# Performance work log

Hardware: AMD Instinct MI355X
Metric: run time of the kernel (lower is better)

Reference implementation:

```python
import jax, jax.numpy as jnp
import numpy as np

N = 50000      # nodes
E = 800000     # edges
IN = 128       # in_channels
HID = 64       # hidden_channels (out per head)
H = 4          # heads
ED = 64        # edge_dim
HC = H * HID   # concat output width


def segment_softmax(logits, seg, num_segments):
    # logits: [E, H], softmax over edges sharing the same destination node
    m = jax.ops.segment_max(logits, seg, num_segments=num_segments)
    m = jnp.where(jnp.isfinite(m), m, 0.0)
    e = jnp.exp(logits - m[seg])
    s = jax.ops.segment_sum(e, seg, num_segments=num_segments)
    return e / (s[seg] + 1e-16)


def gatv2_layer(x, src, dst, edge_attr, Wl, bl, Wr, br, We, att, bias):
    # GATv2Conv (PyG, concat=True, negative_slope=0.2), dropout off (eval)
    Hh, C = att.shape
    xl = (x @ Wl + bl).reshape(-1, Hh, C)   # [N,H,C] source transform
    xr = (x @ Wr + br).reshape(-1, Hh, C)   # [N,H,C] target transform
    ee = (edge_attr @ We).reshape(-1, Hh, C)  # [E,H,C]
    m = jax.nn.leaky_relu(xl[src] + xr[dst] + ee, 0.2)  # [E,H,C]
    logits = jnp.einsum('ehc,hc->eh', m, att)           # [E,H]
    alpha = segment_softmax(logits, dst, x.shape[0])    # [E,H]
    out = jax.ops.segment_sum(alpha[:, :, None] * xl[src], dst,
                              num_segments=x.shape[0])  # [N,H,C]
    return out.reshape(x.shape[0], Hh * C) + bias


def setup_inputs() -> dict:
    key = jax.random.key(0)
    ks = jax.random.split(key, 20)
    g = lambda k, shape, s=0.05: (jax.random.normal(k, shape, jnp.float32) * s)
    inp = {
        'x': jax.random.normal(ks[0], (N, IN), jnp.float32),
        'edge_index': jax.random.randint(ks[1], (2, E), 0, N, dtype=jnp.int32),
        'edge_attr': jax.random.normal(ks[2], (E, ED), jnp.float32),
        # layer 1: in_channels -> heads*hidden
        'Wl1': g(ks[3], (IN, HC)), 'bl1': jnp.zeros((HC,), jnp.float32),
        'Wr1': g(ks[4], (IN, HC)), 'br1': jnp.zeros((HC,), jnp.float32),
        'We1': g(ks[5], (ED, HC)),
        'att1': g(ks[6], (H, HID)), 'bias1': jnp.zeros((HC,), jnp.float32),
        # layer 2: heads*hidden -> heads*hidden
        'Wl2': g(ks[7], (HC, HC)), 'bl2': jnp.zeros((HC,), jnp.float32),
        'Wr2': g(ks[8], (HC, HC)), 'br2': jnp.zeros((HC,), jnp.float32),
        'We2': g(ks[9], (ED, HC)),
        'att2': g(ks[10], (H, HID)), 'bias2': jnp.zeros((HC,), jnp.float32),
    }
    return inp


def reference(x, edge_index, edge_attr,
              Wl1, bl1, Wr1, br1, We1, att1, bias1,
              Wl2, bl2, Wr2, br2, We2, att2, bias2):
    src, dst = edge_index[0], edge_index[1]
    h1 = gatv2_layer(x, src, dst, edge_attr, Wl1, bl1, Wr1, br1, We1, att1, bias1)
    h2 = gatv2_layer(h1, src, dst, edge_attr, Wl2, bl2, Wr2, br2, We2, att2, bias2)
    return h2
```

## Files before the change

kernel.cpp:

```cpp
#include <hip/hip_runtime.h>
#include <math.h>

#define NN 50000
#define NE 800000

#define LRELU(v) fmaxf((v), 0.2f * (v))

typedef __attribute__((ext_vector_type(4))) float f32x4;
typedef __attribute__((ext_vector_type(8))) short bf16x8;

static __device__ __forceinline__ unsigned short f2bf(float f) {
  union { float f; unsigned int i; } c; c.f = f;
  unsigned int r = c.i + 0x7fff + ((c.i >> 16) & 1);
  return (unsigned short)(r >> 16);
}
static __device__ __forceinline__ float bflo(unsigned int u) {
  union { unsigned int i; float f; } c; c.i = u << 16; return c.f;
}
static __device__ __forceinline__ float bfhi(unsigned int u) {
  union { unsigned int i; float f; } c; c.i = u & 0xffff0000u; return c.f;
}

__global__ __launch_bounds__(256)
void conv_all(const float* __restrict__ We1, unsigned short* __restrict__ wef1,
              const float* __restrict__ We2, unsigned short* __restrict__ wef2,
              const float* __restrict__ Wl1, unsigned short* __restrict__ wlf1,
              const float* __restrict__ Wr1, unsigned short* __restrict__ wrf1,
              const float* __restrict__ Wl2, unsigned short* __restrict__ wlf2,
              const float* __restrict__ Wr2, unsigned short* __restrict__ wrf2) {
  const int y = blockIdx.y;
  const int g = blockIdx.x * 256 + threadIdx.x;
  if (y < 2) {
    if (g >= 16384) return;
    const float* We = y ? We2 : We1;
    unsigned short* wef = y ? wef2 : wef1;
    const int j = g & 7;
    const int l = (g >> 3) & 63;
    const int t = g >> 9;
    const int n = t & 15, half = t >> 4;
    const int k = half * 32 + (l >> 4) * 8 + j;
    const int c = ((l & 15) >> 2) * 64 + n * 4 + (l & 3);
    wef[g] = f2bf(We[(size_t)k * 256 + c]);
  } else {
    const int K = (y < 4) ? 128 : 256;
    if (g >= K * 256) return;
    const float* W = (y == 2) ? Wl1 : (y == 3) ? Wr1 : (y == 4) ? Wl2 : Wr2;
    unsigned short* wf = (y == 2) ? wlf1 : (y == 3) ? wrf1
                       : (y == 4) ? wlf2 : wrf2;
    const int j = g & 7;
    const int l = (g >> 3) & 63;
    const int fn = g >> 9;
    const int n = fn & 15, ks = fn >> 4;
    const int k = ks * 32 + (l >> 4) * 8 + j;
    const int c = n * 16 + (l & 15);
    wf[g] = f2bf(W[(size_t)k * 256 + c]);
  }
}

template <int KS, int BF>
__global__ __launch_bounds__(256)
void gemm_mfma4(const void* __restrict__ Av,
                const unsigned short* __restrict__ wf0,
                const float* __restrict__ b0, unsigned short* __restrict__ out0,
                const unsigned short* __restrict__ wf1,
                const float* __restrict__ b1, unsigned short* __restrict__ out1) {
  const int mat = blockIdx.y & 1;
  const int nh  = blockIdx.y >> 1;
  const unsigned short* wf = mat ? wf1 : wf0;
  const float* bias        = mat ? b1 : b0;
  unsigned short* outb     = mat ? out1 : out0;

  const int tid = threadIdx.x;
  const int w = tid >> 6, l = tid & 63;
  const int lid = l & 15, lg = l >> 4;
  const int row  = blockIdx.x * 64 + w * 16 + lid;
  const bool rowok = row < NN;
  const int rowv = rowok ? row : NN - 1;
  const int K = KS * 32;

  bf16x8 bfr[KS];
  if (BF) {
    const unsigned short* A = (const unsigned short*)Av;
    const unsigned short* ap = A + (size_t)rowv * K + lg * 8;
#pragma unroll
    for (int ks = 0; ks < KS; ++ks)
      bfr[ks] = *(const bf16x8*)(ap + ks * 32);
  } else {
    const float* A = (const float*)Av;
    const float* ap = A + (size_t)rowv * K + lg * 8;
#pragma unroll
    for (int ks = 0; ks < KS; ++ks) {
      const float4 v0 = *(const float4*)(ap + ks * 32);
      const float4 v1 = *(const float4*)(ap + ks * 32 + 4);
      bf16x8 b;
      b[0]=f2bf(v0.x); b[1]=f2bf(v0.y); b[2]=f2bf(v0.z); b[3]=f2bf(v0.w);
      b[4]=f2bf(v1.x); b[5]=f2bf(v1.y); b[6]=f2bf(v1.z); b[7]=f2bf(v1.w);
      bfr[ks] = b;
    }
  }

  f32x4 acc[8];
#pragma unroll
  for (int n8 = 0; n8 < 8; ++n8) acc[n8] = (f32x4){0.f, 0.f, 0.f, 0.f};

#pragma unroll
  for (int ks = 0; ks < KS; ++ks)
#pragma unroll
    for (int n8 = 0; n8 < 8; ++n8) {
      const int n = nh * 8 + n8;
      const bf16x8 a = *(const bf16x8*)(wf + ((size_t)(ks * 16 + n) * 64 + l) * 8);
      acc[n8] = __builtin_amdgcn_mfma_f32_16x16x32_bf16(a, bfr[ks], acc[n8], 0, 0, 0);
    }

  if (rowok) {
#pragma unroll
    for (int n8 = 0; n8 < 8; ++n8) {
      const int c0 = (nh * 8 + n8) * 16 + lg * 4;
      const float4 bv = *(const float4*)(bias + c0);
      ushort4 o;
      o.x = f2bf(acc[n8][0] + bv.x); o.y = f2bf(acc[n8][1] + bv.y);
      o.z = f2bf(acc[n8][2] + bv.z); o.w = f2bf(acc[n8][3] + bv.w);
      *(ushort4*)(outb + (size_t)row * 256 + c0) = o;
    }
  }
}

__global__ __launch_bounds__(256)
void dst_hist(const int* __restrict__ dst, int* __restrict__ cnt) {
  const int e = blockIdx.x * 256 + threadIdx.x;
  if (e < NE) atomicAdd(&cnt[dst[e]], 1);
}

__global__ __launch_bounds__(1024)
void scan_bsum(const int* __restrict__ cnt, int* __restrict__ bsum, int n) {
  __shared__ int wsum[16];
  const int tid = threadIdx.x;
  const int lane = tid & 63, wid = tid >> 6;
  const int i = blockIdx.x * 1024 + tid;
  int v = (i < n) ? cnt[i] : 0;
#pragma unroll
  for (int off = 32; off >= 1; off >>= 1) v += __shfl_xor(v, off);
  if (lane == 0) wsum[wid] = v;
  __syncthreads();
  if (tid == 0) {
    int s = 0;
#pragma unroll
    for (int k = 0; k < 16; ++k) s += wsum[k];
    bsum[blockIdx.x] = s;
  }
}

__global__ __launch_bounds__(64)
void scan_bsum_scan(int* __restrict__ bsum, int* __restrict__ row_start,
                    int nb, int n) {
  const int lane = threadIdx.x;
  const int v = (lane < nb) ? bsum[lane] : 0;
  int incl = v;
#pragma unroll
  for (int off = 1; off < 64; off <<= 1) {
    const int t = __shfl_up(incl, off);
    if (lane >= off) incl += t;
  }
  if (lane < nb) bsum[lane] = incl - v;
  if (lane == 63) row_start[n] = incl;
}

__global__ __launch_bounds__(1024)
void scan_apply(int* __restrict__ cnt, const int* __restrict__ bsum,
                int* __restrict__ row_start, int n) {
  __shared__ int wsum[16];
  __shared__ int woff[16];
  const int tid = threadIdx.x;
  const int lane = tid & 63, wid = tid >> 6;
  const int i = blockIdx.x * 1024 + tid;
  const int v = (i < n) ? cnt[i] : 0;
  int incl = v;
#pragma unroll
  for (int off = 1; off < 64; off <<= 1) {
    const int t = __shfl_up(incl, off);
    if (lane >= off) incl += t;
  }
  if (lane == 63) wsum[wid] = incl;
  __syncthreads();
  if (wid == 0) {
    const int s = (lane < 16) ? wsum[lane] : 0;
    int si = s;
#pragma unroll
    for (int off = 1; off < 16; off <<= 1) {
      const int t = __shfl_up(si, off);
      if (lane >= off) si += t;
    }
    if (lane < 16) woff[lane] = si - s;
  }
  __syncthreads();
  if (i < n) {
    const int excl = bsum[blockIdx.x] + woff[wid] + incl - v;
    row_start[i] = excl;
    cnt[i] = excl;
  }
}

__global__ __launch_bounds__(256)
void bucket_fill(const int* __restrict__ src, const int* __restrict__ dst,
                 int* __restrict__ cur, int* __restrict__ eid,
                 int* __restrict__ ssrc, int* __restrict__ sdst) {
  const int e = blockIdx.x * 256 + threadIdx.x;
  if (e < NE) {
    const int d = dst[e];
    const int p = atomicAdd(&cur[d], 1);
    eid[p] = e;
    ssrc[p] = src[e];
    sdst[p] = d;
  }
}

__global__ __launch_bounds__(256)
void conv_eab(const float* __restrict__ ea, const int* __restrict__ eid,
              unsigned short* __restrict__ eab) {
  const int g = blockIdx.x * 256 + threadIdx.x;
  const int p = g >> 4, c4 = (g & 15) * 4;
  const int e = eid[p];
  const float4 v = *(const float4*)(ea + (size_t)e * 64 + c4);
  ushort4 o;
  o.x = f2bf(v.x); o.y = f2bf(v.y); o.z = f2bf(v.z); o.w = f2bf(v.w);
  *(ushort4*)(eab + (size_t)p * 64 + c4) = o;
}

template <int EAB>
__global__ __launch_bounds__(128)
void edge_logits_glds(const float* __restrict__ ea,
                      const unsigned short* __restrict__ eab,
                      const unsigned short* __restrict__ wef,
                      const unsigned short* __restrict__ xlb,
                      const unsigned short* __restrict__ xrb,
                      const float* __restrict__ att,
                      const int* __restrict__ eid,
                      const int* __restrict__ ssrc, const int* __restrict__ sdst,
                      float* __restrict__ elog) {
  __shared__ unsigned short sxl[2][16 * 256];

  const int tid = threadIdx.x;
  const int w = tid >> 6, l = tid & 63;
  const int lid = l & 15, lg = l >> 4;
  const int base = (blockIdx.x * 2 + w) * 16;
  const int p = base + lid;

  const int my_s = ssrc[p];

  const int rr = l >> 5;
  const int u_phys = l & 31;
#pragma unroll
  for (int i = 0; i < 8; ++i) {
    const int r = 2 * i + rr;
    const int srow = __shfl(my_s, r);
    const int u = u_phys ^ (r & 7);
    const unsigned short* gsrc = xlb + (size_t)srow * 256 + u * 8;
    __builtin_amdgcn_global_load_lds(
        (const __attribute__((address_space(1))) unsigned int*)gsrc,
        (__attribute__((address_space(3))) unsigned int*)&sxl[w][i * 512],
        16, 0, 0);
  }

  bf16x8 f0, f1;
  if (EAB) {
    f0 = *(const bf16x8*)(eab + (size_t)p * 64 + lg * 8);
    f1 = *(const bf16x8*)(eab + (size_t)p * 64 + 32 + lg * 8);
  } else {
    const int e = eid[p];
    const float* ap = ea + (size_t)e * 64 + lg * 8;
    const float4 v00 = *(const float4*)(ap);
    const float4 v01 = *(const float4*)(ap + 4);
    const float4 v10 = *(const float4*)(ap + 32);
    const float4 v11 = *(const float4*)(ap + 36);
    f0[0]=f2bf(v00.x); f0[1]=f2bf(v00.y); f0[2]=f2bf(v00.z); f0[3]=f2bf(v00.w);
    f0[4]=f2bf(v01.x); f0[5]=f2bf(v01.y); f0[6]=f2bf(v01.z); f0[7]=f2bf(v01.w);
    f1[0]=f2bf(v10.x); f1[1]=f2bf(v10.y); f1[2]=f2bf(v10.z); f1[3]=f2bf(v10.w);
    f1[4]=f2bf(v11.x); f1[5]=f2bf(v11.y); f1[6]=f2bf(v11.z); f1[7]=f2bf(v11.w);
  }
  const int d = sdst[p];
  const unsigned short* xrp = xrb + (size_t)d * 256 + lg * 64;
  const float* attp = att + lg * 64;
  const unsigned short* xlrow = &sxl[w][lid * 256];
  const int lsw = lid & 7;

  asm volatile("s_waitcnt vmcnt(0)" ::: "memory");
  __builtin_amdgcn_sched_barrier(0);

  float ph = 0.f;
#pragma unroll
  for (int nn = 0; nn < 8; ++nn) {
    const bf16x8 w00 = *(const bf16x8*)(wef + ((size_t)(0  + 2 * nn)     * 64 + l) * 8);
    const bf16x8 w01 = *(const bf16x8*)(wef + ((size_t)(16 + 2 * nn)     * 64 + l) * 8);
    const bf16x8 w10 = *(const bf16x8*)(wef + ((size_t)(0  + 2 * nn + 1) * 64 + l) * 8);
    const bf16x8 w11 = *(const bf16x8*)(wef + ((size_t)(16 + 2 * nn + 1) * 64 + l) * 8);

    f32x4 a0 = (f32x4){0.f,0.f,0.f,0.f}, a1 = (f32x4){0.f,0.f,0.f,0.f};
    a0 = __builtin_amdgcn_mfma_f32_16x16x32_bf16(w00, f0, a0, 0, 0, 0);
    a0 = __builtin_amdgcn_mfma_f32_16x16x32_bf16(w01, f1, a0, 0, 0, 0);
    a1 = __builtin_amdgcn_mfma_f32_16x16x32_bf16(w10, f0, a1, 0, 0, 0);
    a1 = __builtin_amdgcn_mfma_f32_16x16x32_bf16(w11, f1, a1, 0, 0, 0);

    const int up = (lg * 8 + nn) ^ lsw;
    const uint4 xu = *(const uint4*)(xlrow + up * 8);
    const uint4 ru = *(const uint4*)(xrp + nn * 8);
    const float4 at0 = *(const float4*)(attp + nn * 8);
    const float4 at1 = *(const float4*)(attp + nn * 8 + 4);
    float v;
    v = a0[0] + bflo(xu.x) + bflo(ru.x); v = LRELU(v); ph += v * at0.x;
    v = a0[1] + bfhi(xu.x) + bfhi(ru.x); v = LRELU(v); ph += v * at0.y;
    v = a0[2] + bflo(xu.y) + bflo(ru.y); v = LRELU(v); ph += v * at0.z;
    v = a0[3] + bfhi(xu.y) + bfhi(ru.y); v = LRELU(v); ph += v * at0.w;
    v = a1[0] + bflo(xu.z) + bflo(ru.z); v = LRELU(v); ph += v * at1.x;
    v = a1[1] + bfhi(xu.z) + bfhi(ru.z); v = LRELU(v); ph += v * at1.y;
    v = a1[2] + bflo(xu.w) + bflo(ru.w); v = LRELU(v); ph += v * at1.z;
    v = a1[3] + bfhi(xu.w) + bfhi(ru.w); v = LRELU(v); ph += v * at1.w;
  }

  elog[(size_t)p * 4 + lg] = expf(ph);
}

template <int FINAL>
__global__ __launch_bounds__(256)
void aggregate(const unsigned short* __restrict__ xlb,
               const float* __restrict__ elog,
               const int* __restrict__ ssrc, const int* __restrict__ row_start,
               const float* __restrict__ bias, float* __restrict__ outf,
               unsigned short* __restrict__ outb) {
  const int wid  = threadIdx.x >> 6;
  const int lane = threadIdx.x & 63;
  const int d    = blockIdx.x * 4 + wid;
  const int h = lane >> 4;
  const int c = lane * 4;
  float ax = 0.f, ay = 0.f, az = 0.f, aw = 0.f;
  float dtot = 0.f;
  const int beg = row_start[d], end = row_start[d + 1];
  int p = beg;
  for (; p + 4 <= end; p += 4) {
    const float e0 = elog[(size_t)(p + 0) * 4 + h];
    const float e1 = elog[(size_t)(p + 1) * 4 + h];
    const float e2 = elog[(size_t)(p + 2) * 4 + h];
    const float e3 = elog[(size_t)(p + 3) * 4 + h];
    const int s0 = ssrc[p + 0], s1 = ssrc[p + 1];
    const int s2 = ssrc[p + 2], s3 = ssrc[p + 3];
    const uint2 x0 = *(const uint2*)(xlb + (size_t)s0 * 256 + c);
    const uint2 x1 = *(const uint2*)(xlb + (size_t)s1 * 256 + c);
    const uint2 x2 = *(const uint2*)(xlb + (size_t)s2 * 256 + c);
    const uint2 x3 = *(const uint2*)(xlb + (size_t)s3 * 256 + c);
    ax += e0*bflo(x0.x) + e1*bflo(x1.x) + e2*bflo(x2.x) + e3*bflo(x3.x);
    ay += e0*bfhi(x0.x) + e1*bfhi(x1.x) + e2*bfhi(x2.x) + e3*bfhi(x3.x);
    az += e0*bflo(x0.y) + e1*bflo(x1.y) + e2*bflo(x2.y) + e3*bflo(x3.y);
    aw += e0*bfhi(x0.y) + e1*bfhi(x1.y) + e2*bfhi(x2.y) + e3*bfhi(x3.y);
    dtot += e0 + e1 + e2 + e3;
  }
  for (; p < end; ++p) {
    const float ev = elog[(size_t)p * 4 + h];
    const int s = ssrc[p];
    const uint2 xv = *(const uint2*)(xlb + (size_t)s * 256 + c);
    ax += ev * bflo(xv.x); ay += ev * bfhi(xv.x);
    az += ev * bflo(xv.y); aw += ev * bfhi(xv.y);
    dtot += ev;
  }
  const float inv = 1.f / (dtot + 1e-16f);
  const float4 bv = *(const float4*)(bias + c);
  float4 o;
  o.x = bv.x + ax * inv; o.y = bv.y + ay * inv;
  o.z = bv.z + az * inv; o.w = bv.w + aw * inv;
  if (FINAL) {
    *(float4*)(outf + (size_t)d * 256 + c) = o;
  } else {
    ushort4 ob;
    ob.x = f2bf(o.x); ob.y = f2bf(o.y); ob.z = f2bf(o.z); ob.w = f2bf(o.w);
    *(ushort4*)(outb + (size_t)d * 256 + c) = ob;
  }
}

extern "C" void kernel_launch(void* const* d_in, const int* in_sizes, int n_in,
                              void* d_out, int out_size, void* d_ws, size_t ws_size,
                              hipStream_t stream) {
  const float* x    = (const float*)d_in[0];
  const int*   ei   = (const int*)d_in[1];
  const float* ea   = (const float*)d_in[2];
  const float* Wl1  = (const float*)d_in[3];
  const float* bl1  = (const float*)d_in[4];
  const float* Wr1  = (const float*)d_in[5];
  const float* br1  = (const float*)d_in[6];
  const float* We1  = (const float*)d_in[7];
  const float* att1 = (const float*)d_in[8];
  const float* bias1= (const float*)d_in[9];
  const float* Wl2  = (const float*)d_in[10];
  const float* bl2  = (const float*)d_in[11];
  const float* Wr2  = (const float*)d_in[12];
  const float* br2  = (const float*)d_in[13];
  const float* We2  = (const float*)d_in[14];
  const float* att2 = (const float*)d_in[15];
  const float* bias2= (const float*)d_in[16];

  float* out = (float*)d_out;
  float* ws  = (float*)d_ws;

  float* elog = ws;
  unsigned short* xlb  = (unsigned short*)(elog + (size_t)NE * 4);
  unsigned short* xrb  = xlb + (size_t)NN * 256;
  unsigned short* h1b  = xrb + (size_t)NN * 256;
  unsigned short* wef1 = h1b + (size_t)NN * 256;
  unsigned short* wef2 = wef1 + 16384;
  unsigned short* wlf1 = wef2 + 16384;
  unsigned short* wrf1 = wlf1 + 32768;
  unsigned short* wlf2 = wrf1 + 32768;
  unsigned short* wrf2 = wlf2 + 65536;
  int* cur       = (int*)(wrf2 + 65536);
  int* row_start = cur + NN;
  int* bsum      = row_start + NN + 1;
  int* eid       = bsum + 64;
  int* ssrc      = eid + NE;
  int* sdst      = ssrc + NE;
  unsigned short* eab = (unsigned short*)(sdst + NE);
  const size_t need_eab =
      ((char*)(eab + (size_t)NE * 64)) - (char*)d_ws;
  const bool use_eab = ws_size >= need_eab;

  const int* src = ei;
  const int* dst = ei + NE;

  const int ggrid = (NN + 63) / 64;
  const int egrid = NE / 32;
  const int epb   = (NE + 255) / 256;
  const int agrid = NN / 4;
  const int nb    = (NN + 1023) / 1024;

  hipMemsetAsync(cur, 0, NN * sizeof(int), stream);
  conv_all<<<dim3(256, 6), 256, 0, stream>>>(We1, wef1, We2, wef2,
                                             Wl1, wlf1, Wr1, wrf1,
                                             Wl2, wlf2, Wr2, wrf2);
  dst_hist<<<epb, 256, 0, stream>>>(dst, cur);
  scan_bsum<<<nb, 1024, 0, stream>>>(cur, bsum, NN);
  scan_bsum_scan<<<1, 64, 0, stream>>>(bsum, row_start, nb, NN);
  scan_apply<<<nb, 1024, 0, stream>>>(cur, bsum, row_start, NN);
  bucket_fill<<<epb, 256, 0, stream>>>(src, dst, cur, eid, ssrc, sdst);
  if (use_eab)
    conv_eab<<<NE * 16 / 256, 256, 0, stream>>>(ea, eid, eab);

  gemm_mfma4<4, 0><<<dim3(ggrid, 4), 256, 0, stream>>>(x, wlf1, bl1, xlb,
                                                       wrf1, br1, xrb);
  if (use_eab)
    edge_logits_glds<1><<<egrid, 128, 0, stream>>>(ea, eab, wef1, xlb, xrb,
                                                   att1, eid, ssrc, sdst, elog);
  else
    edge_logits_glds<0><<<egrid, 128, 0, stream>>>(ea, eab, wef1, xlb, xrb,
                                                   att1, eid, ssrc, sdst, elog);
  aggregate<0><<<agrid, 256, 0, stream>>>(xlb, elog, ssrc, row_start, bias1,
                                          nullptr, h1b);

  gemm_mfma4<8, 1><<<dim3(ggrid, 4), 256, 0, stream>>>(h1b, wlf2, bl2, xlb,
                                                       wrf2, br2, xrb);
  if (use_eab)
    edge_logits_glds<1><<<egrid, 128, 0, stream>>>(ea, eab, wef2, xlb, xrb,
                                                   att2, eid, ssrc, sdst, elog);
  else
    edge_logits_glds<0><<<egrid, 128, 0, stream>>>(ea, eab, wef2, xlb, xrb,
                                                   att2, eid, ssrc, sdst, elog);
  aggregate<1><<<agrid, 256, 0, stream>>>(xlb, elog, ssrc, row_start, bias2,
                                          out, nullptr);
}
```

Before: 626.0 us.

## Process two 16-edge groups per wave with overlapped LDS gather

Each wave in the edge-logit kernel now handles 32 edges as two groups of 16. Both groups' source-row gathers into LDS (via global_load_lds) are issued up front, and a partial vmcnt wait lets the first group's MFMA epilogue run while the second group's loads are still in flight. The grid is halved to match. The goal is to hide gather latency. In exchange, LDS use per block doubles and register pressure rises, which may lower occupancy.

```diff
diff --git a/kernel.cpp b/kernel.cpp
--- a/kernel.cpp
+++ b/kernel.cpp
@@ -226,66 +226,12 @@
   *(ushort4*)(eab + (size_t)p * 64 + c4) = o;
 }
 
-template <int EAB>
-__global__ __launch_bounds__(128)
-void edge_logits_glds(const float* __restrict__ ea,
-                      const unsigned short* __restrict__ eab,
-                      const unsigned short* __restrict__ wef,
-                      const unsigned short* __restrict__ xlb,
-                      const unsigned short* __restrict__ xrb,
-                      const float* __restrict__ att,
-                      const int* __restrict__ eid,
-                      const int* __restrict__ ssrc, const int* __restrict__ sdst,
-                      float* __restrict__ elog) {
-  __shared__ unsigned short sxl[2][16 * 256];
-
-  const int tid = threadIdx.x;
-  const int w = tid >> 6, l = tid & 63;
-  const int lid = l & 15, lg = l >> 4;
-  const int base = (blockIdx.x * 2 + w) * 16;
-  const int p = base + lid;
-
-  const int my_s = ssrc[p];
-
-  const int rr = l >> 5;
-  const int u_phys = l & 31;
-#pragma unroll
-  for (int i = 0; i < 8; ++i) {
-    const int r = 2 * i + rr;
-    const int srow = __shfl(my_s, r);
-    const int u = u_phys ^ (r & 7);
-    const unsigned short* gsrc = xlb + (size_t)srow * 256 + u * 8;
-    __builtin_amdgcn_global_load_lds(
-        (const __attribute__((address_space(1))) unsigned int*)gsrc,
-        (__attribute__((address_space(3))) unsigned int*)&sxl[w][i * 512],
-        16, 0, 0);
-  }
-
-  bf16x8 f0, f1;
-  if (EAB) {
-    f0 = *(const bf16x8*)(eab + (size_t)p * 64 + lg * 8);
-    f1 = *(const bf16x8*)(eab + (size_t)p * 64 + 32 + lg * 8);
-  } else {
-    const int e = eid[p];
-    const float* ap = ea + (size_t)e * 64 + lg * 8;
-    const float4 v00 = *(const float4*)(ap);
-    const float4 v01 = *(const float4*)(ap + 4);
-    const float4 v10 = *(const float4*)(ap + 32);
-    const float4 v11 = *(const float4*)(ap + 36);
-    f0[0]=f2bf(v00.x); f0[1]=f2bf(v00.y); f0[2]=f2bf(v00.z); f0[3]=f2bf(v00.w);
-    f0[4]=f2bf(v01.x); f0[5]=f2bf(v01.y); f0[6]=f2bf(v01.z); f0[7]=f2bf(v01.w);
-    f1[0]=f2bf(v10.x); f1[1]=f2bf(v10.y); f1[2]=f2bf(v10.z); f1[3]=f2bf(v10.w);
-    f1[4]=f2bf(v11.x); f1[5]=f2bf(v11.y); f1[6]=f2bf(v11.z); f1[7]=f2bf(v11.w);
-  }
-  const int d = sdst[p];
-  const unsigned short* xrp = xrb + (size_t)d * 256 + lg * 64;
-  const float* attp = att + lg * 64;
-  const unsigned short* xlrow = &sxl[w][lid * 256];
-  const int lsw = lid & 7;
-
-  asm volatile("s_waitcnt vmcnt(0)" ::: "memory");
-  __builtin_amdgcn_sched_barrier(0);
-
+static __device__ __forceinline__ float edge_epilogue_sw(
+    const unsigned short* __restrict__ xlrow, int lsw,
+    const unsigned short* __restrict__ xrp,
+    const float* __restrict__ attp,
+    const unsigned short* __restrict__ wef,
+    bf16x8 f0, bf16x8 f1, int l, int lg) {
   float ph = 0.f;
 #pragma unroll
   for (int nn = 0; nn < 8; ++nn) {
@@ -315,8 +261,105 @@
     v = a1[2] + bflo(xu.w) + bflo(ru.w); v = LRELU(v); ph += v * at1.z;
     v = a1[3] + bfhi(xu.w) + bfhi(ru.w); v = LRELU(v); ph += v * at1.w;
   }
-
-  elog[(size_t)p * 4 + lg] = expf(ph);
+  return ph;
+}
+
+template <int EAB>
+__global__ __launch_bounds__(128)
+void edge_logits_glds2(const float* __restrict__ ea,
+                       const unsigned short* __restrict__ eab,
+                       const unsigned short* __restrict__ wef,
+                       const unsigned short* __restrict__ xlb,
+                       const unsigned short* __restrict__ xrb,
+                       const float* __restrict__ att,
+                       const int* __restrict__ eid,
+                       const int* __restrict__ ssrc, const int* __restrict__ sdst,
+                       float* __restrict__ elog) {
+  __shared__ unsigned short sxl[2][2][16 * 256];
+
+  const int tid = threadIdx.x;
+  const int w = tid >> 6, l = tid & 63;
+  const int lid = l & 15, lg = l >> 4;
+  const int base = (blockIdx.x * 2 + w) * 32;
+  const int pA = base + lid;
+  const int pB = base + 16 + lid;
+
+  const int sA_ = ssrc[pA];
+  const int sB_ = ssrc[pB];
+
+  const int rr = l >> 5;
+  const int u_phys = l & 31;
+
+#pragma unroll
+  for (int i = 0; i < 8; ++i) {
+    const int r = 2 * i + rr;
+    const int srow = __shfl(sA_, r);
+    const int u = u_phys ^ (r & 7);
+    __builtin_amdgcn_global_load_lds(
+        (const __attribute__((address_space(1))) unsigned int*)
+            (xlb + (size_t)srow * 256 + u * 8),
+        (__attribute__((address_space(3))) unsigned int*)&sxl[w][0][i * 512],
+        16, 0, 0);
+  }
+  __builtin_amdgcn_sched_barrier(0);
+
+  bf16x8 fA0, fA1, fB0, fB1;
+  if (EAB) {
+    fA0 = *(const bf16x8*)(eab + (size_t)pA * 64 + lg * 8);
+    fA1 = *(const bf16x8*)(eab + (size_t)pA * 64 + 32 + lg * 8);
+    fB0 = *(const bf16x8*)(eab + (size_t)pB * 64 + lg * 8);
+    fB1 = *(const bf16x8*)(eab + (size_t)pB * 64 + 32 + lg * 8);
+  } else {
+    const int eA = eid[pA], eB = eid[pB];
+#pragma unroll
+    for (int g2 = 0; g2 < 2; ++g2) {
+      const float* ap = ea + (size_t)(g2 ? eB : eA) * 64 + lg * 8;
+      const float4 v00 = *(const float4*)(ap);
+      const float4 v01 = *(const float4*)(ap + 4);
+      const float4 v10 = *(const float4*)(ap + 32);
+      const float4 v11 = *(const float4*)(ap + 36);
+      bf16x8 t0, t1;
+      t0[0]=f2bf(v00.x); t0[1]=f2bf(v00.y); t0[2]=f2bf(v00.z); t0[3]=f2bf(v00.w);
+      t0[4]=f2bf(v01.x); t0[5]=f2bf(v01.y); t0[6]=f2bf(v01.z); t0[7]=f2bf(v01.w);
+      t1[0]=f2bf(v10.x); t1[1]=f2bf(v10.y); t1[2]=f2bf(v10.z); t1[3]=f2bf(v10.w);
+      t1[4]=f2bf(v11.x); t1[5]=f2bf(v11.y); t1[6]=f2bf(v11.z); t1[7]=f2bf(v11.w);
+      if (g2) { fB0 = t0; fB1 = t1; } else { fA0 = t0; fA1 = t1; }
+    }
+  }
+  const int dA = sdst[pA];
+  const int dB = sdst[pB];
+  __builtin_amdgcn_sched_barrier(0);
+
+#pragma unroll
+  for (int i = 0; i < 8; ++i) {
+    const int r = 2 * i + rr;
+    const int srow = __shfl(sB_, r);
+    const int u = u_phys ^ (r & 7);
+    __builtin_amdgcn_global_load_lds(
+        (const __attribute__((address_space(1))) unsigned int*)
+            (xlb + (size_t)srow * 256 + u * 8),
+        (__attribute__((address_space(3))) unsigned int*)&sxl[w][1][i * 512],
+        16, 0, 0);
+  }
+  __builtin_amdgcn_sched_barrier(0);
+  asm volatile("s_waitcnt vmcnt(8)" ::: "memory");
+  __builtin_amdgcn_sched_barrier(0);
+
+  const int lsw = lid & 7;
+  const float phA = edge_epilogue_sw(&sxl[w][0][lid * 256], lsw,
+                                     xrb + (size_t)dA * 256 + lg * 64,
+                                     att + lg * 64, wef, fA0, fA1, l, lg);
+  const float evA = expf(phA);
+
+  __builtin_amdgcn_sched_barrier(0);
+  asm volatile("s_waitcnt vmcnt(0)" ::: "memory");
+  __builtin_amdgcn_sched_barrier(0);
+
+  const float phB = edge_epilogue_sw(&sxl[w][1][lid * 256], lsw,
+                                     xrb + (size_t)dB * 256 + lg * 64,
+                                     att + lg * 64, wef, fB0, fB1, l, lg);
+  elog[(size_t)pA * 4 + lg] = evA;
+  elog[(size_t)pB * 4 + lg] = expf(phB);
 }
 
 template <int FINAL>
@@ -423,7 +466,7 @@
   const int* dst = ei + NE;
 
   const int ggrid = (NN + 63) / 64;
-  const int egrid = NE / 32;
+  const int egrid = NE / 64;
   const int epb   = (NE + 255) / 256;
   const int agrid = NN / 4;
   const int nb    = (NN + 1023) / 1024;
@@ -443,22 +486,22 @@
   gemm_mfma4<4, 0><<<dim3(ggrid, 4), 256, 0, stream>>>(x, wlf1, bl1, xlb,
                                                        wrf1, br1, xrb);
   if (use_eab)
-    edge_logits_glds<1><<<egrid, 128, 0, stream>>>(ea, eab, wef1, xlb, xrb,
-                                                   att1, eid, ssrc, sdst, elog);
+    edge_logits_glds2<1><<<egrid, 128, 0, stream>>>(ea, eab, wef1, xlb, xrb,
+                                                    att1, eid, ssrc, sdst, elog);
   else
-    edge_logits_glds<0><<<egrid, 128, 0, stream>>>(ea, eab, wef1, xlb, xrb,
-                                                   att1, eid, ssrc, sdst, elog);
+    edge_logits_glds2<0><<<egrid, 128, 0, stream>>>(ea, eab, wef1, xlb, xrb,
+                                                    att1, eid, ssrc, sdst, elog);
   aggregate<0><<<agrid, 256, 0, stream>>>(xlb, elog, ssrc, row_start, bias1,
                                           nullptr, h1b);
 
   gemm_mfma4<8, 1><<<dim3(ggrid, 4), 256, 0, stream>>>(h1b, wlf2, bl2, xlb,
                                                        wrf2, br2, xrb);
   if (use_eab)
-    edge_logits_glds<1><<<egrid, 128, 0, stream>>>(ea, eab, wef2, xlb, xrb,
-                                                   att2, eid, ssrc, sdst, elog);
+    edge_logits_glds2<1><<<egrid, 128, 0, stream>>>(ea, eab, wef2, xlb, xrb,
+                                                    att2, eid, ssrc, sdst, elog);
   else
-    edge_logits_glds<0><<<egrid, 128, 0, stream>>>(ea, eab, wef2, xlb, xrb,
-                                                   att2, eid, ssrc, sdst, elog);
+    edge_logits_glds2<0><<<egrid, 128, 0, stream>>>(ea, eab, wef2, xlb, xrb,
+                                                    att2, eid, ssrc, sdst, elog);
   aggregate<1><<<agrid, 256, 0, stream>>>(xlb, elog, ssrc, row_start, bias2,
                                           out, nullptr);
 }
```

After: 638.4 us. No clear change (+2.0%).
